# Performance work log

Hardware: AMD Instinct MI355X
Metric: run time of the kernel (lower is better)

## Reference

```python
import jax, jax.numpy as jnp
import numpy as np

KSIZE = 3
SCALE = 2


def setup_inputs() -> dict:
    key = jax.random.key(0)
    k1, k2, k3, k4 = jax.random.split(key, 4)
    B, C, H, W = 8, 3, 512, 512
    h, w = H // SCALE, W // SCALE
    return {
        "images": jax.random.uniform(k1, (B, C, H, W), jnp.float32),
        "kernels": jax.random.uniform(k2, (B, KSIZE ** 2, h, w), jnp.float32),
        "offsets_x": jax.random.uniform(k3, (B, KSIZE ** 2, h, w), jnp.float32),
        "offsets_y": jax.random.uniform(k4, (B, KSIZE ** 2, h, w), jnp.float32),
    }


def _softround(x, alpha=1.0):
    two_pi = 2.0 * jnp.pi
    return x - alpha * (jnp.sin(two_pi * x) / two_pi)


def _batch_bli(im, x, y):
    # im: [B, H, W, 3] channel-last; x, y: [B, N] float coords
    B, N = x.shape
    x0 = jnp.floor(x).astype(jnp.int32)
    x1 = x0 + 1
    y0 = jnp.floor(y).astype(jnp.int32)
    y1 = y0 + 1
    # original clamps x by im.shape[2] and y by im.shape[1] (square images)
    x0 = jnp.clip(x0, 0, im.shape[2] - 1)
    x1 = jnp.clip(x1, 0, im.shape[2] - 1)
    y0 = jnp.clip(y0, 0, im.shape[1] - 1)
    y1 = jnp.clip(y1, 0, im.shape[1] - 1)
    bidx = jnp.arange(B)[:, None]
    # vectorized gather of the four corners; flatten like torch.cat of [3]-vectors
    Ia = im[bidx, x0, y0].reshape(-1)  # [B*N*3]
    Ib = im[bidx, x0, y1].reshape(-1)
    Ic = im[bidx, x1, y0].reshape(-1)
    Id = im[bidx, x1, y1].reshape(-1)
    scale_w = (1.0 / ((x1 - x0) * (y1 - y0))).reshape(-1)  # [B*N]
    # faithful to the original's (scrambling) reshape semantics
    m1 = jnp.concatenate([x1 - x, x - x0], axis=1).astype(jnp.float32)  # [B, 2N]
    m1 = jnp.tile(m1.reshape(B * N, 1, 1, 2), (1, 2, 1, 1))             # [BN,2,1,2]
    m2 = jnp.stack([Ib, Ia, Id, Ic], axis=1).reshape(B * N, 2, 2, 3)    # [BN,2,2,3]
    m3 = jnp.concatenate([y1 - y, y - y0], axis=1).astype(jnp.float32)
    m3 = m3.reshape(B * N, 1, 2, 1)                                     # [BN,1,2,1]
    t = jnp.matmul(m1, m2).transpose(0, 3, 2, 1)  # [BN,3,1,2]
    out = jnp.matmul(t, m3).reshape(B * N, 3)     # [BN,3]
    return scale_w[:, None] * out


def reference(images, kernels, offsets_x, offsets_y):
    B = images.shape[0]
    h, w = images.shape[2] // SCALE, images.shape[3] // SCALE
    kernels = kernels.transpose(0, 2, 3, 1)      # [B,h,w,9]
    ox = offsets_x.transpose(0, 2, 3, 1)         # [B,h,w,9]
    oy = offsets_y.transpose(0, 2, 3, 1)
    u = jnp.arange(h, dtype=jnp.float32) + 0.5 * SCALE - 0.5
    kx = jnp.repeat(jnp.arange(KSIZE), KSIZE).astype(jnp.float32)  # 0,0,0,1,1,1,2,2,2
    ky = jnp.tile(jnp.arange(KSIZE), KSIZE).astype(jnp.float32)    # 0,1,2,0,1,2,0,1,2
    # original broadcasts u.reshape(h,1) over the w axis (requires h == w)
    coords_x = ox + KSIZE / 2 + kx + u[:, None]
    coords_y = oy + KSIZE / 2 + ky + u[:, None]
    im = images.transpose(0, 2, 3, 1)  # [B,H,W,3]
    pix = _batch_bli(im, coords_x.reshape(B, -1), coords_y.reshape(B, -1))
    pix_hr = pix.reshape(B, h, w, KSIZE ** 2, 3)
    out = jnp.sum(kernels[..., None] * pix_hr, axis=-2)  # [B,h,w,3]
    return _softround(out * 255.0)
```

## Files before the change

kernel.cpp:

```cpp
#include <hip/hip_runtime.h>
#include <math.h>

#define BATCH 8
#define HI 512
#define WI 512
#define HO 256
#define WO 256
#define PLANE (HI*WI)
#define OPIX (HO*WO)
#define LROWS 68
#define LCOLS 10
#define LSTRIDE 33
#define LDS_FLOATS (LROWS*LSTRIDE)

__global__ __launch_bounds__(256) void downsampler_kernel(
    const float* __restrict__ images,
    const float* __restrict__ kernels,
    const float* __restrict__ offx,
    const float* __restrict__ offy,
    float* __restrict__ out)
{
    __shared__ float simg[LDS_FLOATS];

    const int blk = blockIdx.x;
    const int b    = blk >> 8;
    const int ihx  = (blk >> 2) & 63;
    const int w0   = (blk & 3) << 6;
    const int tid  = threadIdx.x;
    const int iw   = w0 + (tid & 63);
    const int ih   = (ihx << 2) + (tid >> 6);

    {
        const float* imb = images + (size_t)b * 3 * PLANE;
        const int total = LROWS * LCOLS * 3;
        for (int i = tid; i < total; i += 256) {
            const int ch  = i / (LROWS * LCOLS);
            const int rem = i - ch * (LROWS * LCOLS);
            const int rr  = rem / LCOLS;
            const int cr  = rem - rr * LCOLS;
            const int r = w0 + 2 + rr;
            int c = r - 4 + cr;
            c = c < 0 ? 0 : (c > WI - 1 ? WI - 1 : c);
            simg[rr * LSTRIDE + cr * 3 + ch] = imb[ch * PLANE + r * WI + c];
        }
    }
    __syncthreads();

    const int pl  = ih * WO + iw;
    const int pl2 = (2 * pl) & (OPIX - 1);
    const bool flip = (pl < (OPIX / 2));

    const float* offxb = offx    + (size_t)b * 9 * OPIX;
    const float* offyb = offy    + (size_t)b * 9 * OPIX;
    const float* kernb = kernels + (size_t)b * 9 * OPIX;

    const float uu_own = (float)iw + 0.5f;
    const float uu_s0 = (float)((2 * iw) & (WO - 1)) + 0.5f;
    const float uu_s1 = (float)((2 * iw + 1) & (WO - 1)) + 0.5f;

    float acc0 = 0.f, acc1 = 0.f, acc2 = 0.f;

    #pragma unroll
    for (int k = 0; k < 9; ++k) {
        const float kxf = (float)(k / 3);
        const float kyf = (float)(k - 3 * (k / 3));
        const float cx = ((offxb[k * OPIX + pl] + 1.5f) + kxf) + uu_own;
        const float cy = ((offyb[k * OPIX + pl] + 1.5f) + kyf) + uu_own;
        const int x0 = (int)floorf(cx);
        const int y0 = (int)floorf(cy);

        const int ta = 2 * k;
        const int tb = 2 * k + 1;
        const int sel_a = (ta >= 9) ? 1 : 0;
        const int sel_b = (tb >= 9) ? 1 : 0;
        const int ks_a = ta - 9 * sel_a;
        const int ks_b = tb - 9 * sel_b;
        const float uu_a = sel_a ? uu_s1 : uu_s0;
        const float uu_b = sel_b ? uu_s1 : uu_s0;
        const float kxa = (float)(ks_a / 3), kya = (float)(ks_a - 3 * (ks_a / 3));
        const float kxb = (float)(ks_b / 3), kyb = (float)(ks_b - 3 * (ks_b / 3));

        const float cxa = ((offxb[ks_a * OPIX + pl2 + sel_a] + 1.5f) + kxa) + uu_a;
        const float cya = ((offyb[ks_a * OPIX + pl2 + sel_a] + 1.5f) + kya) + uu_a;
        const float cxb = ((offxb[ks_b * OPIX + pl2 + sel_b] + 1.5f) + kxb) + uu_b;
        const float cyb = ((offyb[ks_b * OPIX + pl2 + sel_b] + 1.5f) + kyb) + uu_b;

        const float fxa = cxa - floorf(cxa);
        const float fya = cya - floorf(cya);
        const float fxb = cxb - floorf(cxb);
        const float fyb = cyb - floorf(cyb);
        const float w0w = flip ? (1.0f - fxa) : fxa;
        const float w1w = flip ? (1.0f - fxb) : fxb;
        const float v0w = flip ? (1.0f - fya) : fya;
        const float v1w = flip ? (1.0f - fyb) : fyb;

        const float* r0 = &simg[(x0 - 2 - w0) * LSTRIDE];
        const float* r1 = r0 + LSTRIDE;
        const int c00 = (y0 - x0 + 4) * 3;
        const int c01 = c00 + 3;
        const int c10 = c00 - 3;
        const int c11 = c00;

        const float Ia0 = r0[c00 + 0], Ia1 = r0[c00 + 1], Ia2 = r0[c00 + 2];
        const float Ib0 = r0[c01 + 0], Ib1 = r0[c01 + 1], Ib2 = r0[c01 + 2];
        const float Ic0 = r1[c10 + 0], Ic1 = r1[c10 + 1], Ic2 = r1[c10 + 2];
        const float Id0 = r1[c11 + 0], Id1 = r1[c11 + 1], Id2 = r1[c11 + 2];

        const float w0v0 = w0w * v0w, w1v0 = w1w * v0w;
        const float w0v1 = w0w * v1w, w1v1 = w1w * v1w;

        const float p0 = w0v0 * Ib0 + w1v0 * Ic0 + w0v1 * Id1 + w1v1 * Ia2;
        const float p1 = w0v0 * Ia0 + w1v0 * Ib1 + w0v1 * Ic1 + w1v1 * Id2;
        const float p2 = w0v0 * Id0 + w1v0 * Ia1 + w0v1 * Ib2 + w1v1 * Ic2;

        const float kv = kernb[k * OPIX + pl];
        acc0 += kv * p0;
        acc1 += kv * p1;
        acc2 += kv * p2;
    }

    const float TWO_PI     = 6.28318530717958647692f;
    const float INV_TWO_PI = 0.15915494309189533577f;
    const size_t obase = ((size_t)b * OPIX + (size_t)pl) * 3;
    const float z0 = acc0 * 255.0f;
    const float z1 = acc1 * 255.0f;
    const float z2 = acc2 * 255.0f;
    out[obase + 0] = z0 - sinf(TWO_PI * z0) * INV_TWO_PI;
    out[obase + 1] = z1 - sinf(TWO_PI * z1) * INV_TWO_PI;
    out[obase + 2] = z2 - sinf(TWO_PI * z2) * INV_TWO_PI;
}

extern "C" void kernel_launch(void* const* d_in, const int* in_sizes, int n_in,
                              void* d_out, int out_size, void* d_ws, size_t ws_size,
                              hipStream_t stream) {
    const float* images  = (const float*)d_in[0];
    const float* kernels = (const float*)d_in[1];
    const float* offx    = (const float*)d_in[2];
    const float* offy    = (const float*)d_in[3];
    float* out = (float*)d_out;

    dim3 grid(BATCH * 64 * 4);
    dim3 block(256);
    hipLaunchKernelGGL(downsampler_kernel, grid, block, 0, stream,
                       images, kernels, offx, offy, out);
}
```

Before: 120.1 us.

## Process two output rows per thread with vectorized offset loads and hardware sine

Each thread now computes two output rows, so the grid shrinks by half and each block's shared-memory image tile load serves twice as many pixels. The scrambled-offset reads become float2 vector loads, and their interpolation weights are computed up front into register arrays. The softround sine is replaced by range reduction with rintf plus the hardware sin builtin, which takes its argument in revolutions. Other changes are a launch-bounds occupancy hint and dropping the upper clamp on the tile column. The risks are higher register pressure from the 18-entry weight arrays, and small precision differences from the hardware sine.

Measured after the change: 116.2 us. -3.2%, faster.

```diff
diff --git a/kernel.cpp b/kernel.cpp
--- a/kernel.cpp
+++ b/kernel.cpp
@@ -13,7 +13,7 @@
 #define LSTRIDE 33
 #define LDS_FLOATS (LROWS*LSTRIDE)
 
-__global__ __launch_bounds__(256) void downsampler_kernel(
+__global__ __launch_bounds__(256, 4) void downsampler_kernel(
     const float* __restrict__ images,
     const float* __restrict__ kernels,
     const float* __restrict__ offx,
@@ -22,13 +22,14 @@
 {
     __shared__ float simg[LDS_FLOATS];
 
-    const int blk = blockIdx.x;
-    const int b    = blk >> 8;
-    const int ihx  = (blk >> 2) & 63;
+    const int blk  = blockIdx.x;
+    const int b    = blk >> 7;
+    const int ihx  = (blk >> 2) & 31;
     const int w0   = (blk & 3) << 6;
     const int tid  = threadIdx.x;
-    const int iw   = w0 + (tid & 63);
-    const int ih   = (ihx << 2) + (tid >> 6);
+    const int lane = tid & 63;
+    const int g    = tid >> 6;
+    const int iw   = w0 + lane;
 
     {
         const float* imb = images + (size_t)b * 3 * PLANE;
@@ -40,94 +41,101 @@
             const int cr  = rem - rr * LCOLS;
             const int r = w0 + 2 + rr;
             int c = r - 4 + cr;
-            c = c < 0 ? 0 : (c > WI - 1 ? WI - 1 : c);
+            c = c < 0 ? 0 : c;
             simg[rr * LSTRIDE + cr * 3 + ch] = imb[ch * PLANE + r * WI + c];
         }
     }
     __syncthreads();
 
-    const int pl  = ih * WO + iw;
-    const int pl2 = (2 * pl) & (OPIX - 1);
-    const bool flip = (pl < (OPIX / 2));
-
+    const bool flip = (ihx < 16);
     const float* offxb = offx    + (size_t)b * 9 * OPIX;
     const float* offyb = offy    + (size_t)b * 9 * OPIX;
     const float* kernb = kernels + (size_t)b * 9 * OPIX;
 
     const float uu_own = (float)iw + 0.5f;
-    const float uu_s0 = (float)((2 * iw) & (WO - 1)) + 0.5f;
-    const float uu_s1 = (float)((2 * iw + 1) & (WO - 1)) + 0.5f;
+    const float uu_s0  = (float)((2 * iw) & 255) + 0.5f;
+    const float uu_s1  = uu_s0 + 1.0f;
 
-    float acc0 = 0.f, acc1 = 0.f, acc2 = 0.f;
+    const float TWO_PI_INV = 0.15915494309189533577f;
 
     #pragma unroll
-    for (int k = 0; k < 9; ++k) {
-        const float kxf = (float)(k / 3);
-        const float kyf = (float)(k - 3 * (k / 3));
-        const float cx = ((offxb[k * OPIX + pl] + 1.5f) + kxf) + uu_own;
-        const float cy = ((offyb[k * OPIX + pl] + 1.5f) + kyf) + uu_own;
-        const int x0 = (int)floorf(cx);
-        const int y0 = (int)floorf(cy);
+    for (int p = 0; p < 2; ++p) {
+        const int ih = (ihx << 3) + (g << 1) + p;
+        const int pl = ih * WO + iw;
+        const int pix2 = pl & (OPIX / 2 - 1);
 
-        const int ta = 2 * k;
-        const int tb = 2 * k + 1;
-        const int sel_a = (ta >= 9) ? 1 : 0;
-        const int sel_b = (tb >= 9) ? 1 : 0;
-        const int ks_a = ta - 9 * sel_a;
-        const int ks_b = tb - 9 * sel_b;
-        const float uu_a = sel_a ? uu_s1 : uu_s0;
-        const float uu_b = sel_b ? uu_s1 : uu_s0;
-        const float kxa = (float)(ks_a / 3), kya = (float)(ks_a - 3 * (ks_a / 3));
-        const float kxb = (float)(ks_b / 3), kyb = (float)(ks_b - 3 * (ks_b / 3));
+        float2 vx[9], vy[9];
+        #pragma unroll
+        for (int ks = 0; ks < 9; ++ks) {
+            vx[ks] = ((const float2*)(offxb + ks * OPIX))[pix2];
+            vy[ks] = ((const float2*)(offyb + ks * OPIX))[pix2];
+        }
+        float wx[18], wy[18];
+        #pragma unroll
+        for (int t = 0; t < 18; ++t) {
+            const int sel = (t >= 9) ? 1 : 0;
+            const int ks  = t - 9 * sel;
+            const float uu  = sel ? uu_s1 : uu_s0;
+            const float oxv = sel ? vx[ks].y : vx[ks].x;
+            const float oyv = sel ? vy[ks].y : vy[ks].x;
+            const float kxf = (float)(ks / 3);
+            const float kyf = (float)(ks - 3 * (ks / 3));
+            const float cxx = ((oxv + 1.5f) + kxf) + uu;
+            const float cyy = ((oyv + 1.5f) + kyf) + uu;
+            const float fx = cxx - floorf(cxx);
+            const float fy = cyy - floorf(cyy);
+            wx[t] = flip ? (1.0f - fx) : fx;
+            wy[t] = flip ? (1.0f - fy) : fy;
+        }
 
-        const float cxa = ((offxb[ks_a * OPIX + pl2 + sel_a] + 1.5f) + kxa) + uu_a;
-        const float cya = ((offyb[ks_a * OPIX + pl2 + sel_a] + 1.5f) + kya) + uu_a;
-        const float cxb = ((offxb[ks_b * OPIX + pl2 + sel_b] + 1.5f) + kxb) + uu_b;
-        const float cyb = ((offyb[ks_b * OPIX + pl2 + sel_b] + 1.5f) + kyb) + uu_b;
+        float acc0 = 0.f, acc1 = 0.f, acc2 = 0.f;
+        #pragma unroll
+        for (int k = 0; k < 9; ++k) {
+            const float kxf = (float)(k / 3);
+            const float kyf = (float)(k - 3 * (k / 3));
+            const float cx = ((offxb[k * OPIX + pl] + 1.5f) + kxf) + uu_own;
+            const float cy = ((offyb[k * OPIX + pl] + 1.5f) + kyf) + uu_own;
+            const int x0 = (int)floorf(cx);
+            const int y0 = (int)floorf(cy);
 
-        const float fxa = cxa - floorf(cxa);
-        const float fya = cya - floorf(cya);
-        const float fxb = cxb - floorf(cxb);
-        const float fyb = cyb - floorf(cyb);
-        const float w0w = flip ? (1.0f - fxa) : fxa;
-        const float w1w = flip ? (1.0f - fxb) : fxb;
-        const float v0w = flip ? (1.0f - fya) : fya;
-        const float v1w = flip ? (1.0f - fyb) : fyb;
+            const float* r0 = &simg[(x0 - 2 - w0) * LSTRIDE];
+            const float* r1 = r0 + LSTRIDE;
+            const int c00 = (y0 - x0 + 4) * 3;
+            const int c01 = c00 + 3;
+            const int c10 = c00 - 3;
+            const int c11 = c00;
 
-        const float* r0 = &simg[(x0 - 2 - w0) * LSTRIDE];
-        const float* r1 = r0 + LSTRIDE;
-        const int c00 = (y0 - x0 + 4) * 3;
-        const int c01 = c00 + 3;
-        const int c10 = c00 - 3;
-        const int c11 = c00;
+            const float Ia0 = r0[c00 + 0], Ia1 = r0[c00 + 1], Ia2 = r0[c00 + 2];
+            const float Ib0 = r0[c01 + 0], Ib1 = r0[c01 + 1], Ib2 = r0[c01 + 2];
+            const float Ic0 = r1[c10 + 0], Ic1 = r1[c10 + 1], Ic2 = r1[c10 + 2];
+            const float Id0 = r1[c11 + 0], Id1 = r1[c11 + 1], Id2 = r1[c11 + 2];
 
-        const float Ia0 = r0[c00 + 0], Ia1 = r0[c00 + 1], Ia2 = r0[c00 + 2];
-        const float Ib0 = r0[c01 + 0], Ib1 = r0[c01 + 1], Ib2 = r0[c01 + 2];
-        const float Ic0 = r1[c10 + 0], Ic1 = r1[c10 + 1], Ic2 = r1[c10 + 2];
-        const float Id0 = r1[c11 + 0], Id1 = r1[c11 + 1], Id2 = r1[c11 + 2];
+            const float w0w = wx[2 * k], w1w = wx[2 * k + 1];
+            const float v0w = wy[2 * k], v1w = wy[2 * k + 1];
+            const float w0v0 = w0w * v0w, w1v0 = w1w * v0w;
+            const float w0v1 = w0w * v1w, w1v1 = w1w * v1w;
 
-        const float w0v0 = w0w * v0w, w1v0 = w1w * v0w;
-        const float w0v1 = w0w * v1w, w1v1 = w1w * v1w;
+            const float p0 = w0v0 * Ib0 + w1v0 * Ic0 + w0v1 * Id1 + w1v1 * Ia2;
+            const float p1 = w0v0 * Ia0 + w1v0 * Ib1 + w0v1 * Ic1 + w1v1 * Id2;
+            const float p2 = w0v0 * Id0 + w1v0 * Ia1 + w0v1 * Ib2 + w1v1 * Ic2;
 
-        const float p0 = w0v0 * Ib0 + w1v0 * Ic0 + w0v1 * Id1 + w1v1 * Ia2;
-        const float p1 = w0v0 * Ia0 + w1v0 * Ib1 + w0v1 * Ic1 + w1v1 * Id2;
-        const float p2 = w0v0 * Id0 + w1v0 * Ia1 + w0v1 * Ib2 + w1v1 * Ic2;
+            const float kv = kernb[k * OPIX + pl];
+            acc0 += kv * p0;
+            acc1 += kv * p1;
+            acc2 += kv * p2;
+        }
 
-        const float kv = kernb[k * OPIX + pl];
-        acc0 += kv * p0;
-        acc1 += kv * p1;
-        acc2 += kv * p2;
+        const size_t obase = ((size_t)b * OPIX + (size_t)pl) * 3;
+        const float z0 = acc0 * 255.0f;
+        const float z1 = acc1 * 255.0f;
+        const float z2 = acc2 * 255.0f;
+        const float r0s = z0 - rintf(z0);
+        const float r1s = z1 - rintf(z1);
+        const float r2s = z2 - rintf(z2);
+        out[obase + 0] = z0 - __builtin_amdgcn_sinf(r0s) * TWO_PI_INV;
+        out[obase + 1] = z1 - __builtin_amdgcn_sinf(r1s) * TWO_PI_INV;
+        out[obase + 2] = z2 - __builtin_amdgcn_sinf(r2s) * TWO_PI_INV;
     }
-
-    const float TWO_PI     = 6.28318530717958647692f;
-    const float INV_TWO_PI = 0.15915494309189533577f;
-    const size_t obase = ((size_t)b * OPIX + (size_t)pl) * 3;
-    const float z0 = acc0 * 255.0f;
-    const float z1 = acc1 * 255.0f;
-    const float z2 = acc2 * 255.0f;
-    out[obase + 0] = z0 - sinf(TWO_PI * z0) * INV_TWO_PI;
-    out[obase + 1] = z1 - sinf(TWO_PI * z1) * INV_TWO_PI;
-    out[obase + 2] = z2 - sinf(TWO_PI * z2) * INV_TWO_PI;
 }
 
 extern "C" void kernel_launch(void* const* d_in, const int* in_sizes, int n_in,
@@ -139,7 +147,7 @@
     const float* offy    = (const float*)d_in[3];
     float* out = (float*)d_out;
 
-    dim3 grid(BATCH * 64 * 4);
+    dim3 grid(BATCH * 32 * 4);
     dim3 block(256);
     hipLaunchKernelGGL(downsampler_kernel, grid, block, 0, stream,
                        images, kernels, offx, offy, out);
```
